# Performance work log

Hardware: AMD Instinct MI355X
Metric: run time of the kernel (lower is better)

The kernel has to match this reference:

```python
import jax, jax.numpy as jnp
import numpy as np

S, E, C = 8192, 64, 256  # tokens, experts, capacity


def setup_inputs() -> dict:
    key = jax.random.key(0)
    k1, k2, k3, k4 = jax.random.split(key, 4)
    logits = jax.random.normal(k1, (S, E), dtype=jnp.float32)
    # top-2 expert assignment (mask2 is the second choice, disjoint from mask1)
    top1 = jnp.argmax(logits, axis=1)
    mask1 = jax.nn.one_hot(top1, E, dtype=jnp.float32)
    masked = logits - mask1 * 1e9
    top2 = jnp.argmax(masked, axis=1)
    mask2 = jax.nn.one_hot(top2, E, dtype=jnp.float32)
    # one-hot capacity slot encodings [s, c]
    loc1 = jax.nn.one_hot(jax.random.randint(k3, (S,), 0, C), C, dtype=jnp.float32)
    loc2 = jax.nn.one_hot(jax.random.randint(k4, (S,), 0, C), C, dtype=jnp.float32)
    return {
        "logits": logits,
        "mask1_float": mask1,
        "mask2_float": mask2,
        "locations1_sc": loc1,
        "locations2_sc": loc2,
    }


def reference(logits, mask1_float, mask2_float, locations1_sc, locations2_sc):
    gates = jax.nn.softmax(logits, axis=1)                      # [s, e]
    num_experts = gates.shape[1]
    me = jnp.mean(gates, axis=0)                                # [e]
    ce = jnp.mean(mask1_float, axis=0)                          # [e]
    l_aux = jnp.mean(me * ce) * num_experts * num_experts
    gates1_s = jnp.einsum('se,se->s', gates, mask1_float)       # [s]
    gates2_s = jnp.einsum('se,se->s', gates, mask2_float)       # [s]
    denom_s = gates1_s + gates2_s
    denom_s = jnp.maximum(denom_s, jnp.finfo(denom_s.dtype).eps)
    gates1_s = gates1_s / denom_s
    gates2_s = gates2_s / denom_s
    gates1 = gates1_s[:, None] * mask1_float                    # [s, e]
    gates2 = gates2_s[:, None] * mask2_float                    # [s, e]
    combine1_sec = jnp.einsum('se,sc->sec', gates1, locations1_sc)
    combine2_sec = jnp.einsum('se,sc->sec', gates2, locations2_sc)
    combine_weights = combine1_sec + combine2_sec               # [s, e, c]
    return (l_aux, combine_weights)
```

## Files before the change

### kernel.cpp

```cpp
#include <hip/hip_runtime.h>
#include <hip/hip_bf16.h>
#include <float.h>

constexpr int S = 8192;
constexpr int E = 64;
constexpr int C = 256;
constexpr int EC = E * C;
constexpr int PRE_BLOCKS = 512;
constexpr int FILL_BLOCKS = 8192;
constexpr size_t WS_PARTIALS_OFF = (size_t)S * 4;

typedef float f32x4 __attribute__((ext_vector_type(4)));

__global__ __launch_bounds__(256) void mega_kernel(
        const float* __restrict__ logits,
        const float* __restrict__ mask1,
        const float* __restrict__ mask2,
        const float* __restrict__ loc1,
        const float* __restrict__ loc2,
        float4* __restrict__ recs,
        float* __restrict__ ws_partials,
        float* __restrict__ out) {
    __shared__ float me_s[4][64];
    __shared__ float ce_s[4][64];

    if (blockIdx.x >= PRE_BLOCKS) {
        const unsigned blk = blockIdx.x - PRE_BLOCKS;
        f32x4* __restrict__ p = reinterpret_cast<f32x4*>(out) +
                                (size_t)blk * 4096 + threadIdx.x;
        const f32x4 z = {0.f, 0.f, 0.f, 0.f};
        #pragma unroll
        for (int k = 0; k < 16; ++k)
            __builtin_nontemporal_store(z, p + (k << 8));
        if (blk == 0 && threadIdx.x == 0)
            out[(size_t)S * EC] = 0.f;
        return;
    }

    const int lane = threadIdx.x & 63;
    const int wave = threadIdx.x >> 6;

    float me_acc = 0.f, ce_acc = 0.f;

    #pragma unroll
    for (int r = 0; r < 4; ++r) {
        const int s = blockIdx.x * 16 + wave * 4 + r;

        const float x = logits[(size_t)s * E + lane];
        float mx = x;
        #pragma unroll
        for (int off = 32; off > 0; off >>= 1) mx = fmaxf(mx, __shfl_xor(mx, off));
        const float ex = __expf(x - mx);
        float sum = ex;
        #pragma unroll
        for (int off = 32; off > 0; off >>= 1) sum += __shfl_xor(sum, off);
        const float g = ex / sum;

        const float m1v = mask1[(size_t)s * E + lane];
        const float m2v = mask2[(size_t)s * E + lane];
        me_acc += g;
        ce_acc += m1v;

        const int e1 = __ffsll(__ballot(m1v > 0.5f)) - 1;
        const int e2 = __ffsll(__ballot(m2v > 0.5f)) - 1;
        const float g1 = __shfl(g, e1);
        const float g2 = __shfl(g, e2);

        const float4 l1v = *reinterpret_cast<const float4*>(loc1 + (size_t)s * C + lane * 4);
        const float4 l2v = *reinterpret_cast<const float4*>(loc2 + (size_t)s * C + lane * 4);
        const int bm1 = (l1v.x > 0.5f ? 1 : 0) | (l1v.y > 0.5f ? 2 : 0) |
                        (l1v.z > 0.5f ? 4 : 0) | (l1v.w > 0.5f ? 8 : 0);
        const int bm2 = (l2v.x > 0.5f ? 1 : 0) | (l2v.y > 0.5f ? 2 : 0) |
                        (l2v.z > 0.5f ? 4 : 0) | (l2v.w > 0.5f ? 8 : 0);
        const int L1 = __ffsll(__ballot(bm1 != 0)) - 1;
        const int L2 = __ffsll(__ballot(bm2 != 0)) - 1;
        const int c1 = L1 * 4 + (__ffs(__shfl(bm1, L1)) - 1);
        const int c2 = L2 * 4 + (__ffs(__shfl(bm2, L2)) - 1);

        if (lane == 0) {
            const float denom = fmaxf(g1 + g2, FLT_EPSILON);
            float4 rec;
            rec.x = g1 / denom;
            rec.y = g2 / denom;
            rec.z = __int_as_float(e1 * C + c1);
            rec.w = __int_as_float(e2 * C + c2);
            recs[s] = rec;
        }
    }

    me_s[wave][lane] = me_acc;
    ce_s[wave][lane] = ce_acc;
    __syncthreads();
    if (threadIdx.x < 64) {
        const float me_b = me_s[0][lane] + me_s[1][lane] + me_s[2][lane] + me_s[3][lane];
        const float ce_b = ce_s[0][lane] + ce_s[1][lane] + ce_s[2][lane] + ce_s[3][lane];
        ws_partials[(size_t)blockIdx.x * 128 + lane]      = me_b;
        ws_partials[(size_t)blockIdx.x * 128 + 64 + lane] = ce_b;
    }
}

__global__ __launch_bounds__(256) void finalize_kernel(
        const float4* __restrict__ recs,
        const float* __restrict__ ws_partials,
        float* __restrict__ out) {
    if (blockIdx.x < 32) {
        const int t = blockIdx.x * 256 + threadIdx.x;
        const float4 rec = recs[t];
        float* __restrict__ base = out + 1 + (size_t)t * EC;
        base[__float_as_int(rec.z)] = rec.x;
        base[__float_as_int(rec.w)] = rec.y;
    } else {
        __shared__ float mes[4][64];
        __shared__ float ces[4][64];
        const int e = threadIdx.x & 63;
        const int q = threadIdx.x >> 6;
        float me = 0.f, ce = 0.f;
        for (int b = q; b < PRE_BLOCKS; b += 4) {
            me += ws_partials[(size_t)b * 128 + e];
            ce += ws_partials[(size_t)b * 128 + 64 + e];
        }
        mes[q][e] = me;
        ces[q][e] = ce;
        __syncthreads();
        if (threadIdx.x < 64) {
            const float m = mes[0][e] + mes[1][e] + mes[2][e] + mes[3][e];
            const float c = ces[0][e] + ces[1][e] + ces[2][e] + ces[3][e];
            float prod = m * c;
            #pragma unroll
            for (int off = 32; off > 0; off >>= 1) prod += __shfl_xor(prod, off);
            if (e == 0) out[0] = prod * (float)E / ((float)S * (float)S);
        }
    }
}

extern "C" void kernel_launch(void* const* d_in, const int* in_sizes, int n_in,
                              void* d_out, int out_size, void* d_ws, size_t ws_size,
                              hipStream_t stream) {
    const float* logits = (const float*)d_in[0];
    const float* mask1  = (const float*)d_in[1];
    const float* mask2  = (const float*)d_in[2];
    const float* loc1   = (const float*)d_in[3];
    const float* loc2   = (const float*)d_in[4];
    float* out = (float*)d_out;
    float* ws  = (float*)d_ws;

    float4* recs        = (float4*)ws;
    float*  ws_partials = ws + WS_PARTIALS_OFF;

    mega_kernel<<<PRE_BLOCKS + FILL_BLOCKS, 256, 0, stream>>>(
        logits, mask1, mask2, loc1, loc2, recs, ws_partials, out);

    finalize_kernel<<<33, 256, 0, stream>>>(recs, ws_partials, out);
}
```

Measured before the change: 142.2 us.

## Merge zero-fill into uniform grid-stride blocks that also do per-token routing

Replaces the split grid (512 compute blocks plus 8192 dedicated fill blocks) with 2048 uniform blocks. Each block handles one token per wave, then zero-fills the 512 MiB output with a grid-stride loop of plain (not nontemporal) vector stores. The goal is to overlap the routing loads with the dominant fill traffic and to drop the many tiny fill blocks. The trade-offs are that the nontemporal store hint is gone and that the per-block partial sums now cover 2048 blocks, so finalize has to read four times as many partials.

Measured after the change: 304.0 us. +113.9%, slower.

```diff
diff --git a/kernel.cpp b/kernel.cpp
--- a/kernel.cpp
+++ b/kernel.cpp
@@ -6,8 +6,11 @@
 constexpr int E = 64;
 constexpr int C = 256;
 constexpr int EC = E * C;
-constexpr int PRE_BLOCKS = 512;
-constexpr int FILL_BLOCKS = 8192;
+constexpr int MEGA_BLOCKS = 2048;
+constexpr unsigned THREADS = 256u;
+constexpr unsigned TOTAL_THR = MEGA_BLOCKS * THREADS;
+constexpr unsigned N4 = 33554432u;
+constexpr int FILL_ITERS = N4 / TOTAL_THR;
 constexpr size_t WS_PARTIALS_OFF = (size_t)S * 4;
 
 typedef float f32x4 __attribute__((ext_vector_type(4)));
@@ -24,72 +27,51 @@
     __shared__ float me_s[4][64];
     __shared__ float ce_s[4][64];
 
-    if (blockIdx.x >= PRE_BLOCKS) {
-        const unsigned blk = blockIdx.x - PRE_BLOCKS;
-        f32x4* __restrict__ p = reinterpret_cast<f32x4*>(out) +
-                                (size_t)blk * 4096 + threadIdx.x;
-        const f32x4 z = {0.f, 0.f, 0.f, 0.f};
-        #pragma unroll
-        for (int k = 0; k < 16; ++k)
-            __builtin_nontemporal_store(z, p + (k << 8));
-        if (blk == 0 && threadIdx.x == 0)
-            out[(size_t)S * EC] = 0.f;
-        return;
+    const int lane = threadIdx.x & 63;
+    const int wave = threadIdx.x >> 6;
+    const int s    = blockIdx.x * 4 + wave;
+
+    const float x   = logits[(size_t)s * E + lane];
+    const float m1v = mask1[(size_t)s * E + lane];
+    const float m2v = mask2[(size_t)s * E + lane];
+    const float4 l1v = *reinterpret_cast<const float4*>(loc1 + (size_t)s * C + lane * 4);
+    const float4 l2v = *reinterpret_cast<const float4*>(loc2 + (size_t)s * C + lane * 4);
+
+    float mx = x;
+    #pragma unroll
+    for (int off = 32; off > 0; off >>= 1) mx = fmaxf(mx, __shfl_xor(mx, off));
+    const float ex = __expf(x - mx);
+    float sum = ex;
+    #pragma unroll
+    for (int off = 32; off > 0; off >>= 1) sum += __shfl_xor(sum, off);
+    const float g = ex / sum;
+
+    const int e1 = __ffsll(__ballot(m1v > 0.5f)) - 1;
+    const int e2 = __ffsll(__ballot(m2v > 0.5f)) - 1;
+    const float g1 = __shfl(g, e1);
+    const float g2 = __shfl(g, e2);
+
+    const int bm1 = (l1v.x > 0.5f ? 1 : 0) | (l1v.y > 0.5f ? 2 : 0) |
+                    (l1v.z > 0.5f ? 4 : 0) | (l1v.w > 0.5f ? 8 : 0);
+    const int bm2 = (l2v.x > 0.5f ? 1 : 0) | (l2v.y > 0.5f ? 2 : 0) |
+                    (l2v.z > 0.5f ? 4 : 0) | (l2v.w > 0.5f ? 8 : 0);
+    const int L1 = __ffsll(__ballot(bm1 != 0)) - 1;
+    const int L2 = __ffsll(__ballot(bm2 != 0)) - 1;
+    const int c1 = L1 * 4 + (__ffs(__shfl(bm1, L1)) - 1);
+    const int c2 = L2 * 4 + (__ffs(__shfl(bm2, L2)) - 1);
+
+    if (lane == 0) {
+        const float denom = fmaxf(g1 + g2, FLT_EPSILON);
+        float4 rec;
+        rec.x = g1 / denom;
+        rec.y = g2 / denom;
+        rec.z = __int_as_float(e1 * C + c1);
+        rec.w = __int_as_float(e2 * C + c2);
+        recs[s] = rec;
     }
 
-    const int lane = threadIdx.x & 63;
-    const int wave = threadIdx.x >> 6;
-
-    float me_acc = 0.f, ce_acc = 0.f;
-
-    #pragma unroll
-    for (int r = 0; r < 4; ++r) {
-        const int s = blockIdx.x * 16 + wave * 4 + r;
-
-        const float x = logits[(size_t)s * E + lane];
-        float mx = x;
-        #pragma unroll
-        for (int off = 32; off > 0; off >>= 1) mx = fmaxf(mx, __shfl_xor(mx, off));
-        const float ex = __expf(x - mx);
-        float sum = ex;
-        #pragma unroll
-        for (int off = 32; off > 0; off >>= 1) sum += __shfl_xor(sum, off);
-        const float g = ex / sum;
-
-        const float m1v = mask1[(size_t)s * E + lane];
-        const float m2v = mask2[(size_t)s * E + lane];
-        me_acc += g;
-        ce_acc += m1v;
-
-        const int e1 = __ffsll(__ballot(m1v > 0.5f)) - 1;
-        const int e2 = __ffsll(__ballot(m2v > 0.5f)) - 1;
-        const float g1 = __shfl(g, e1);
-        const float g2 = __shfl(g, e2);
-
-        const float4 l1v = *reinterpret_cast<const float4*>(loc1 + (size_t)s * C + lane * 4);
-        const float4 l2v = *reinterpret_cast<const float4*>(loc2 + (size_t)s * C + lane * 4);
-        const int bm1 = (l1v.x > 0.5f ? 1 : 0) | (l1v.y > 0.5f ? 2 : 0) |
-                        (l1v.z > 0.5f ? 4 : 0) | (l1v.w > 0.5f ? 8 : 0);
-        const int bm2 = (l2v.x > 0.5f ? 1 : 0) | (l2v.y > 0.5f ? 2 : 0) |
-                        (l2v.z > 0.5f ? 4 : 0) | (l2v.w > 0.5f ? 8 : 0);
-        const int L1 = __ffsll(__ballot(bm1 != 0)) - 1;
-        const int L2 = __ffsll(__ballot(bm2 != 0)) - 1;
-        const int c1 = L1 * 4 + (__ffs(__shfl(bm1, L1)) - 1);
-        const int c2 = L2 * 4 + (__ffs(__shfl(bm2, L2)) - 1);
-
-        if (lane == 0) {
-            const float denom = fmaxf(g1 + g2, FLT_EPSILON);
-            float4 rec;
-            rec.x = g1 / denom;
-            rec.y = g2 / denom;
-            rec.z = __int_as_float(e1 * C + c1);
-            rec.w = __int_as_float(e2 * C + c2);
-            recs[s] = rec;
-        }
-    }
-
-    me_s[wave][lane] = me_acc;
-    ce_s[wave][lane] = ce_acc;
+    me_s[wave][lane] = g;
+    ce_s[wave][lane] = m1v;
     __syncthreads();
     if (threadIdx.x < 64) {
         const float me_b = me_s[0][lane] + me_s[1][lane] + me_s[2][lane] + me_s[3][lane];
@@ -97,6 +79,14 @@
         ws_partials[(size_t)blockIdx.x * 128 + lane]      = me_b;
         ws_partials[(size_t)blockIdx.x * 128 + 64 + lane] = ce_b;
     }
+
+    f32x4* __restrict__ p = reinterpret_cast<f32x4*>(out);
+    const unsigned gtid = blockIdx.x * THREADS + threadIdx.x;
+    const f32x4 z = {0.f, 0.f, 0.f, 0.f};
+    #pragma unroll 8
+    for (int it = 0; it < FILL_ITERS; ++it)
+        p[(size_t)gtid + (size_t)it * TOTAL_THR] = z;
+    if (gtid == 0) out[(size_t)S * EC] = 0.f;
 }
 
 __global__ __launch_bounds__(256) void finalize_kernel(
@@ -115,7 +105,7 @@
         const int e = threadIdx.x & 63;
         const int q = threadIdx.x >> 6;
         float me = 0.f, ce = 0.f;
-        for (int b = q; b < PRE_BLOCKS; b += 4) {
+        for (int b = q; b < MEGA_BLOCKS; b += 4) {
             me += ws_partials[(size_t)b * 128 + e];
             ce += ws_partials[(size_t)b * 128 + 64 + e];
         }
@@ -147,7 +137,7 @@
     float4* recs        = (float4*)ws;
     float*  ws_partials = ws + WS_PARTIALS_OFF;
 
-    mega_kernel<<<PRE_BLOCKS + FILL_BLOCKS, 256, 0, stream>>>(
+    mega_kernel<<<MEGA_BLOCKS, THREADS, 0, stream>>>(
         logits, mask1, mask2, loc1, loc2, recs, ws_partials, out);
 
     finalize_kernel<<<33, 256, 0, stream>>>(recs, ws_partials, out);
```
